# Performance work log

Measured on AMD Instinct MI355X. Metric: run time of the kernel, lower is better.

Reference implementation:

```python
import jax, jax.numpy as jnp
import numpy as np

N_NODES = 10000
N_EDGES = 640000
CH = 128


def setup_inputs() -> dict:
    key = jax.random.key(0)
    ks = jax.random.split(key, 12)
    inp = {
        "node_feat": jax.random.normal(ks[0], (N_NODES, 118), dtype=jnp.float32),
        "edge_feat": jax.random.normal(ks[1], (N_EDGES, 22), dtype=jnp.float32),
        "src": jax.random.randint(ks[2], (N_EDGES,), 0, N_NODES),
        "dst": jax.random.randint(ks[3], (N_EDGES,), 0, N_NODES),
        "W_node": jax.random.normal(ks[4], (118, CH), dtype=jnp.float32) * 0.05,
        "b_node": jax.random.normal(ks[5], (CH,), dtype=jnp.float32) * 0.05,
        "W_edge": jax.random.normal(ks[6], (22, CH), dtype=jnp.float32) * 0.05,
        "b_edge": jax.random.normal(ks[7], (CH,), dtype=jnp.float32) * 0.05,
        "W_a1": jax.random.normal(ks[8], (2 * CH, CH), dtype=jnp.float32) * 0.05,
        "b_a1": jax.random.normal(ks[9], (CH,), dtype=jnp.float32) * 0.05,
        "W_a2": jax.random.normal(ks[10], (CH, 1), dtype=jnp.float32) * 0.05,
        "b_a2": jax.random.normal(ks[11], (1,), dtype=jnp.float32) * 0.05,
        "layer_num": 3,
    }
    return inp


def reference(node_feat, edge_feat, src, dst, W_node, b_node, W_edge, b_edge,
              W_a1, b_a1, W_a2, b_a2, layer_num):
    # node_map / edge_map (apply_nodes / apply_edges)
    h = node_feat @ W_node + b_node          # [N, C] node hidden
    eh = edge_feat @ W_edge + b_edge         # [E, C] edge hidden (stored on graph, unused by attn)
    e = None
    for _ in range(layer_num):
        # per-edge gather of src/dst hidden, concat -> small 2-layer MLP
        cat = jnp.concatenate([h[src], h[dst]], axis=-1)   # [E, 2C]
        x = jax.nn.leaky_relu(cat @ W_a1 + b_a1)           # torch default slope 0.01
        e = x @ W_a2 + b_a2                                # [E, 1]
    return e
```

## Files before the change

### kernel.cpp

```cpp
#include <hip/hip_runtime.h>
#include <hip/hip_bf16.h>

#define N_NODES 10000
#define N_EDGES 640000
#define CH 128
#define KN 118

typedef _Float16 h2 __attribute__((ext_vector_type(2)));
typedef _Float16 h8 __attribute__((ext_vector_type(8)));

#define H2_OF(v, k) __builtin_shufflevector((v), (v), 2 * (k), 2 * (k) + 1)

__global__ __launch_bounds__(128) void k1_weights(
    const float* __restrict__ Wn, const float* __restrict__ bn,
    const float* __restrict__ Wa1, const float* __restrict__ ba1,
    const float* __restrict__ w2, float* __restrict__ M,
    float* __restrict__ V, _Float16* __restrict__ w2h) {
  int c = threadIdx.x;
  int mat = blockIdx.x / 119;
  int i = blockIdx.x % 119;
  if (mat == 2) {
    w2h[c] = (_Float16)w2[c];
    return;
  }
  const float* B = Wa1 + mat * CH * CH;
  const float* a = (i < KN) ? (Wn + i * CH) : bn;
  float acc = 0.f;
#pragma unroll 8
  for (int j = 0; j < CH; ++j) acc = fmaf(a[j], B[j * CH + c], acc);
  if (i < KN) {
    M[(mat * KN + i) * CH + c] = acc;
  } else {
    if (mat == 1) acc += ba1[c];
    V[mat * CH + c] = acc;
  }
}

__global__ __launch_bounds__(256) void k2_nodes(
    const float* __restrict__ nf, const float* __restrict__ M,
    const float* __restrict__ V, _Float16* __restrict__ T) {
  int tx = threadIdx.x;
  int c = tx & (CH - 1);
  int mat = tx >> 7;
  int n0 = blockIdx.x * 8;
  const float* Mm = M + mat * KN * CH + c;
  const float* r = nf + (size_t)n0 * KN;
  float acc[8];
#pragma unroll
  for (int j = 0; j < 8; ++j) acc[j] = 0.f;
#pragma unroll 2
  for (int k = 0; k < KN; ++k) {
    float m = Mm[k * CH];
#pragma unroll
    for (int j = 0; j < 8; ++j) acc[j] = fmaf(r[j * KN + k], m, acc[j]);
  }
  float v = V[mat * CH + c];
  _Float16* t = T + (size_t)mat * N_NODES * CH + c;
#pragma unroll
  for (int j = 0; j < 8; ++j)
    t[(size_t)(n0 + j) * CH] = (_Float16)(acc[j] + v);
}

__device__ inline float edge_acc8(h8 s, h8 d, h8 w) {
  h8 t = s + d;
  h8 p = t * (_Float16)0.01f;
  h8 u = __builtin_elementwise_max(t, p);
  float acc = 0.f;
  acc = __builtin_amdgcn_fdot2(H2_OF(u, 0), H2_OF(w, 0), acc, false);
  acc = __builtin_amdgcn_fdot2(H2_OF(u, 1), H2_OF(w, 1), acc, false);
  acc = __builtin_amdgcn_fdot2(H2_OF(u, 2), H2_OF(w, 2), acc, false);
  acc = __builtin_amdgcn_fdot2(H2_OF(u, 3), H2_OF(w, 3), acc, false);
  return acc;
}

__global__ __launch_bounds__(256) void k3_edges(
    const int* __restrict__ src, const int* __restrict__ dst,
    const _Float16* __restrict__ S, const _Float16* __restrict__ D,
    const _Float16* __restrict__ w2h, const float* __restrict__ b2,
    float* __restrict__ out) {
  int tid = blockIdx.x * 256 + threadIdx.x;
  int g = tid >> 4;
  int sub = tid & 15;
  int c0 = sub << 3;

  h8 w = *(const h8*)(w2h + c0);
  int4 s4 = *(const int4*)(src + 4 * g);
  int4 d4 = *(const int4*)(dst + 4 * g);

  const _Float16* Sp = S + c0;
  const _Float16* Dp = D + c0;
  h8 sr0 = *(const h8*)(Sp + ((size_t)s4.x << 7));
  h8 dr0 = *(const h8*)(Dp + ((size_t)d4.x << 7));
  h8 sr1 = *(const h8*)(Sp + ((size_t)s4.y << 7));
  h8 dr1 = *(const h8*)(Dp + ((size_t)d4.y << 7));
  h8 sr2 = *(const h8*)(Sp + ((size_t)s4.z << 7));
  h8 dr2 = *(const h8*)(Dp + ((size_t)d4.z << 7));
  h8 sr3 = *(const h8*)(Sp + ((size_t)s4.w << 7));
  h8 dr3 = *(const h8*)(Dp + ((size_t)d4.w << 7));

  float a0 = edge_acc8(sr0, dr0, w);
  float a1 = edge_acc8(sr1, dr1, w);
  float a2 = edge_acc8(sr2, dr2, w);
  float a3 = edge_acc8(sr3, dr3, w);

  float r0 = a0 + __shfl_xor(a0, 1);
  float r1 = a1 + __shfl_xor(a1, 1);
  float r2 = a2 + __shfl_xor(a2, 1);
  float r3 = a3 + __shfl_xor(a3, 1);
  float v1 = (sub & 1) ? r1 : r0;
  float v2 = (sub & 1) ? r3 : r2;
  float t1 = v1 + __shfl_xor(v1, 2);
  float t2 = v2 + __shfl_xor(v2, 2);
  float u = (sub & 2) ? t2 : t1;
  u += __shfl_xor(u, 4);
  u += __shfl_xor(u, 8);

  if (sub < 4) out[4 * g + sub] = u + b2[0];
}

extern "C" void kernel_launch(void* const* d_in, const int* in_sizes, int n_in,
                              void* d_out, int out_size, void* d_ws, size_t ws_size,
                              hipStream_t stream) {
  const float* nf  = (const float*)d_in[0];
  const int*   src = (const int*)d_in[2];
  const int*   dst = (const int*)d_in[3];
  const float* Wn  = (const float*)d_in[4];
  const float* bn  = (const float*)d_in[5];
  const float* Wa1 = (const float*)d_in[8];
  const float* ba1 = (const float*)d_in[9];
  const float* Wa2 = (const float*)d_in[10];
  const float* ba2 = (const float*)d_in[11];
  float* out = (float*)d_out;

  char* ws = (char*)d_ws;
  float* M = (float*)ws;
  float* V = (float*)(ws + 2 * KN * CH * sizeof(float));
  _Float16* w2h = (_Float16*)(ws + (2 * KN * CH + 2 * CH) * sizeof(float));
  _Float16* T = (_Float16*)((char*)w2h + CH * sizeof(_Float16));
  _Float16* S = T;
  _Float16* D = T + (size_t)N_NODES * CH;

  k1_weights<<<239, 128, 0, stream>>>(Wn, bn, Wa1, ba1, Wa2, M, V, w2h);
  k2_nodes<<<N_NODES / 8, 256, 0, stream>>>(nf, M, V, T);
  k3_edges<<<(N_EDGES / 4 * 16) / 256, 256, 0, stream>>>(src, dst, S, D, w2h, ba2, out);
}
```

Baseline: 163.8 us.

## Split edge gather into two channel-half passes with partial-sum buffer

Node tables are stored as two 64-channel halves so that each edge pass gathers from a smaller table (about 2.5 MB instead of 5 MB in fp16), which should fit better in cache. The edge kernel runs twice, once per half, and the second pass adds the partial result of the first plus the bias. The node kernel also processes 16 nodes per block instead of 8. The cost is reading src/dst twice and an extra partial-sum write and read.

```diff
diff --git a/kernel.cpp b/kernel.cpp
--- a/kernel.cpp
+++ b/kernel.cpp
@@ -42,23 +42,25 @@
   int tx = threadIdx.x;
   int c = tx & (CH - 1);
   int mat = tx >> 7;
-  int n0 = blockIdx.x * 8;
+  int n0 = blockIdx.x * 16;
   const float* Mm = M + mat * KN * CH + c;
   const float* r = nf + (size_t)n0 * KN;
-  float acc[8];
+  float acc[16];
 #pragma unroll
-  for (int j = 0; j < 8; ++j) acc[j] = 0.f;
+  for (int j = 0; j < 16; ++j) acc[j] = 0.f;
 #pragma unroll 2
   for (int k = 0; k < KN; ++k) {
     float m = Mm[k * CH];
 #pragma unroll
-    for (int j = 0; j < 8; ++j) acc[j] = fmaf(r[j * KN + k], m, acc[j]);
+    for (int j = 0; j < 16; ++j) acc[j] = fmaf(r[j * KN + k], m, acc[j]);
   }
   float v = V[mat * CH + c];
-  _Float16* t = T + (size_t)mat * N_NODES * CH + c;
+  int half = c >> 6;
+  int cc = c & 63;
+  _Float16* t = T + ((size_t)half * 2 + mat) * N_NODES * 64 + cc;
 #pragma unroll
-  for (int j = 0; j < 8; ++j)
-    t[(size_t)(n0 + j) * CH] = (_Float16)(acc[j] + v);
+  for (int j = 0; j < 16; ++j)
+    t[(size_t)(n0 + j) * 64] = (_Float16)(acc[j] + v);
 }
 
 __device__ inline float edge_acc8(h8 s, h8 d, h8 w) {
@@ -73,49 +75,52 @@
   return acc;
 }
 
-__global__ __launch_bounds__(256) void k3_edges(
+__global__ __launch_bounds__(256) void k3_half(
     const int* __restrict__ src, const int* __restrict__ dst,
-    const _Float16* __restrict__ S, const _Float16* __restrict__ D,
-    const _Float16* __restrict__ w2h, const float* __restrict__ b2,
-    float* __restrict__ out) {
+    const _Float16* __restrict__ Sh, const _Float16* __restrict__ Dh,
+    const _Float16* __restrict__ w2h, const float* __restrict__ partial,
+    const float* __restrict__ b2, float* __restrict__ outp, int fin) {
   int tid = blockIdx.x * 256 + threadIdx.x;
-  int g = tid >> 4;
-  int sub = tid & 15;
+  int g = tid >> 3;
+  int sub = tid & 7;
   int c0 = sub << 3;
 
   h8 w = *(const h8*)(w2h + c0);
   int4 s4 = *(const int4*)(src + 4 * g);
   int4 d4 = *(const int4*)(dst + 4 * g);
 
-  const _Float16* Sp = S + c0;
-  const _Float16* Dp = D + c0;
-  h8 sr0 = *(const h8*)(Sp + ((size_t)s4.x << 7));
-  h8 dr0 = *(const h8*)(Dp + ((size_t)d4.x << 7));
-  h8 sr1 = *(const h8*)(Sp + ((size_t)s4.y << 7));
-  h8 dr1 = *(const h8*)(Dp + ((size_t)d4.y << 7));
-  h8 sr2 = *(const h8*)(Sp + ((size_t)s4.z << 7));
-  h8 dr2 = *(const h8*)(Dp + ((size_t)d4.z << 7));
-  h8 sr3 = *(const h8*)(Sp + ((size_t)s4.w << 7));
-  h8 dr3 = *(const h8*)(Dp + ((size_t)d4.w << 7));
+  const _Float16* Sp = Sh + c0;
+  const _Float16* Dp = Dh + c0;
+  h8 s0 = *(const h8*)(Sp + ((size_t)s4.x << 6));
+  h8 d0 = *(const h8*)(Dp + ((size_t)d4.x << 6));
+  h8 s1 = *(const h8*)(Sp + ((size_t)s4.y << 6));
+  h8 d1 = *(const h8*)(Dp + ((size_t)d4.y << 6));
+  h8 s2 = *(const h8*)(Sp + ((size_t)s4.z << 6));
+  h8 d2 = *(const h8*)(Dp + ((size_t)d4.z << 6));
+  h8 s3 = *(const h8*)(Sp + ((size_t)s4.w << 6));
+  h8 d3 = *(const h8*)(Dp + ((size_t)d4.w << 6));
 
-  float a0 = edge_acc8(sr0, dr0, w);
-  float a1 = edge_acc8(sr1, dr1, w);
-  float a2 = edge_acc8(sr2, dr2, w);
-  float a3 = edge_acc8(sr3, dr3, w);
+  float a0 = edge_acc8(s0, d0, w);
+  float a1 = edge_acc8(s1, d1, w);
+  float a2 = edge_acc8(s2, d2, w);
+  float a3 = edge_acc8(s3, d3, w);
 
   float r0 = a0 + __shfl_xor(a0, 1);
   float r1 = a1 + __shfl_xor(a1, 1);
   float r2 = a2 + __shfl_xor(a2, 1);
   float r3 = a3 + __shfl_xor(a3, 1);
-  float v1 = (sub & 1) ? r1 : r0;
-  float v2 = (sub & 1) ? r3 : r2;
+  float v0 = (sub & 1) ? r1 : r0;
+  float v1 = (sub & 1) ? r3 : r2;
+  float t0 = v0 + __shfl_xor(v0, 2);
   float t1 = v1 + __shfl_xor(v1, 2);
-  float t2 = v2 + __shfl_xor(v2, 2);
-  float u = (sub & 2) ? t2 : t1;
+  float u = (sub & 2) ? t1 : t0;
   u += __shfl_xor(u, 4);
-  u += __shfl_xor(u, 8);
 
-  if (sub < 4) out[4 * g + sub] = u + b2[0];
+  if (sub < 4) {
+    int e = 4 * g + sub;
+    if (fin) u += partial[e] + b2[0];
+    outp[e] = u;
+  }
 }
 
 extern "C" void kernel_launch(void* const* d_in, const int* in_sizes, int n_in,
@@ -137,10 +142,15 @@
   float* V = (float*)(ws + 2 * KN * CH * sizeof(float));
   _Float16* w2h = (_Float16*)(ws + (2 * KN * CH + 2 * CH) * sizeof(float));
   _Float16* T = (_Float16*)((char*)w2h + CH * sizeof(_Float16));
-  _Float16* S = T;
-  _Float16* D = T + (size_t)N_NODES * CH;
+  _Float16* S0 = T;
+  _Float16* D0 = T + (size_t)N_NODES * 64;
+  _Float16* S1 = T + (size_t)2 * N_NODES * 64;
+  _Float16* D1 = T + (size_t)3 * N_NODES * 64;
+  float* P = (float*)(T + (size_t)4 * N_NODES * 64);
 
   k1_weights<<<239, 128, 0, stream>>>(Wn, bn, Wa1, ba1, Wa2, M, V, w2h);
-  k2_nodes<<<N_NODES / 8, 256, 0, stream>>>(nf, M, V, T);
-  k3_edges<<<(N_EDGES / 4 * 16) / 256, 256, 0, stream>>>(src, dst, S, D, w2h, ba2, out);
+  k2_nodes<<<N_NODES / 16, 256, 0, stream>>>(nf, M, V, T);
+  const int k3_blocks = (N_EDGES / 4 * 8) / 256;
+  k3_half<<<k3_blocks, 256, 0, stream>>>(src, dst, S0, D0, w2h, P, ba2, P, 0);
+  k3_half<<<k3_blocks, 256, 0, stream>>>(src, dst, S1, D1, w2h + 64, P, ba2, out, 1);
 }
```

New measurement: 170.1 us. 3.8% more time.
